# Performance work log

Hardware: AMD Instinct MI355X
Metric: run time of the kernel (lower is better)

## Reference

```python
import jax, jax.numpy as jnp
import numpy as np

B, C, H, W = 16, 64, 64, 64
HEADS = 8

def conv1x1(x, w):
    # x: [B, Cin, H, W], w: [Cout, Cin] -> [B, Cout, H, W]
    return jnp.einsum('oc,bchw->bohw', w, x)

def maxpool2x2(x):
    b, c, h, w = x.shape
    return x.reshape(b, c, h // 2, 2, w // 2, 2).max(axis=(3, 5))

def setup_inputs() -> dict:
    key = jax.random.key(0)
    ks = jax.random.split(key, 6)
    x = jax.random.normal(ks[0], (B, C, H, W), dtype=jnp.float32)
    w_theta = jax.random.normal(ks[1], (C // HEADS, C), dtype=jnp.float32) * 0.05
    w_phi = jax.random.normal(ks[2], (C // HEADS, C), dtype=jnp.float32) * 0.05
    w_g = jax.random.normal(ks[3], (C // 2, C), dtype=jnp.float32) * 0.05
    w_o = jax.random.normal(ks[4], (C, C // 2), dtype=jnp.float32) * 0.05
    gamma = jax.random.normal(ks[5], (), dtype=jnp.float32)
    return {'x': x, 'w_theta': w_theta, 'w_phi': w_phi, 'w_g': w_g, 'w_o': w_o, 'gamma': gamma}

def reference(x, w_theta, w_phi, w_g, w_o, gamma):
    b, c, h, w = x.shape
    n = h * w                      # query length
    m = n // 4                     # kv length after 2x2 maxpool
    theta = conv1x1(x, w_theta).reshape(b, c // HEADS, n)   # [B, C/h, N]
    phi = maxpool2x2(conv1x1(x, w_phi)).reshape(b, c // HEADS, m)  # [B, C/h, M]
    g = maxpool2x2(conv1x1(x, w_g)).reshape(b, c // 2, m)   # [B, C/2, M]
    # attention: theta^T @ phi -> [B, N, M]; NOTE: no 1/sqrt(d) scaling (SAGAN)
    beta = jax.nn.softmax(jnp.einsum('bdn,bdm->bnm', theta, phi), axis=-1)
    # o = g @ beta^T -> [B, C/2, N]
    o = jnp.einsum('bdm,bnm->bdn', g, beta).reshape(b, c // 2, h, w)
    o = conv1x1(o, w_o)            # [B, C, H, W]
    return gamma * o + x
```

## Files before the change

### kernel.cpp

```cpp
#include <hip/hip_runtime.h>
#include <hip/hip_bf16.h>

#define NB 16
#define NC 64
#define NN 4096
#define NM 1024
#define ND 8
#define NG 32

typedef short short8 __attribute__((ext_vector_type(8)));
typedef float floatx4 __attribute__((ext_vector_type(4)));

#define LOG2E 1.44269504f

__device__ __forceinline__ short f2bfs(float f) {
    union { __hip_bfloat16 h; short s; } u;
    u.h = __float2bfloat16(f);
    return u.s;
}
__device__ __forceinline__ unsigned pack2bf(float a, float b) {
    return (unsigned)(unsigned short)f2bfs(a) | ((unsigned)(unsigned short)f2bfs(b) << 16);
}
__device__ __forceinline__ unsigned pk2fast(float a, float b) {
    unsigned ua = __float_as_uint(a) + 0x8000u;
    unsigned ub = __float_as_uint(b) + 0x8000u;
    return __builtin_amdgcn_perm(ub, ua, 0x07060302);
}
__device__ __forceinline__ short8 u4s8(uint4 v) {
    union { uint4 u; short8 s; } c; c.u = v; return c.s;
}

__device__ __forceinline__ uint4 ld_coh(const unsigned* base, size_t u4idx) {
    const unsigned long long* p = (const unsigned long long*)base + u4idx * 2;
    unsigned long long lo = __hip_atomic_load(p,     __ATOMIC_RELAXED,
                                              __HIP_MEMORY_SCOPE_SYSTEM);
    unsigned long long hi = __hip_atomic_load(p + 1, __ATOMIC_RELAXED,
                                              __HIP_MEMORY_SCOPE_SYSTEM);
    return make_uint4((unsigned)lo, (unsigned)(lo >> 32),
                      (unsigned)hi, (unsigned)(hi >> 32));
}
__device__ __forceinline__ void st_coh(unsigned* base, size_t u4idx, uint4 v) {
    unsigned long long* p = (unsigned long long*)base + u4idx * 2;
    __hip_atomic_store(p,     (unsigned long long)v.x | ((unsigned long long)v.y << 32),
                       __ATOMIC_RELAXED, __HIP_MEMORY_SCOPE_SYSTEM);
    __hip_atomic_store(p + 1, (unsigned long long)v.z | ((unsigned long long)v.w << 32),
                       __ATOMIC_RELAXED, __HIP_MEMORY_SCOPE_SYSTEM);
}

#define KG_STEP(CPP0, CPP1, CG_)                                                         \
    {                                                                                    \
        _Pragma("unroll")                                                                \
        for (int qt = 0; qt < 2; ++qt) {                                                 \
            floatx4 s0 = __builtin_amdgcn_mfma_f32_16x16x32_bf16(                        \
                u4s8(CPP0), u4s8(tb[qt]), (floatx4)0.f, 0, 0, 0);                        \
            floatx4 s1 = __builtin_amdgcn_mfma_f32_16x16x32_bf16(                        \
                u4s8(CPP1), u4s8(tb[qt]), (floatx4)0.f, 0, 0, 0);                        \
            float e0[4], e1[4];                                                          \
            _Pragma("unroll")                                                            \
            for (int r = 0; r < 4; ++r) {                                                \
                e0[r] = __builtin_amdgcn_exp2f(s0[r]);                                   \
                e1[r] = __builtin_amdgcn_exp2f(s1[r]);                                   \
            }                                                                            \
            lsum[qt] += ((e0[0] + e0[1]) + (e0[2] + e0[3]))                              \
                      + ((e1[0] + e1[1]) + (e1[2] + e1[3]));                             \
            uint4 pb = make_uint4(pk2fast(e0[0], e0[1]), pk2fast(e0[2], e0[3]),          \
                                  pk2fast(e1[0], e1[1]), pk2fast(e1[2], e1[3]));         \
            _Pragma("unroll")                                                            \
            for (int ct = 0; ct < 4; ++ct)                                               \
                acc[qt][ct] = __builtin_amdgcn_mfma_f32_16x16x32_bf16(                   \
                    u4s8(CG_[ct]), u4s8(pb), acc[qt][ct], 0, 0, 0);                      \
        }                                                                                \
    }

__global__ void init_flags(int* __restrict__ flags)
{
    flags[threadIdx.x] = 0;
}

__global__ __launch_bounds__(256, 2)
void fused_kernel(const float* __restrict__ x,
                  const float* __restrict__ w_theta,
                  const float* __restrict__ w_phi,
                  const float* __restrict__ w_g,
                  const float* __restrict__ w_o,
                  const float* __restrict__ gamma_p,
                  unsigned* __restrict__ phi_ws,
                  unsigned* __restrict__ g2_ws,
                  int* __restrict__ flags,
                  float* __restrict__ out)
{
    __shared__ __align__(16) float smem[16096];
    float* lx   = smem;
    float* lwpT = smem + 8448;
    float* lwgT = smem + 8960;
    float* lwoT = smem + 11072;
    float* lgs  = smem + 13152;
    float* lps  = smem + 14304;
    float* lwt  = smem + 14560;
    float* lth  = smem + 15072;
    uint4* lphi = (uint4*)(smem + 8960);
    uint4* lg2  = (uint4*)(smem + 13056);
    float* ltr  = smem;

    const int blk  = blockIdx.x;
    const int xcd  = blk & 7;
    const int slot = blk >> 3;
    const int b    = xcd * 2 + (slot >> 5);
    const int ph   = slot & 31;
    const int t    = threadIdx.x;
    const int w    = t >> 6;
    const int lane = t & 63;
    const int lm   = lane & 15;
    const int quad = lane >> 4;

    for (int i = t; i < 512; i += 256) {
        lwpT[(i & 63) * 8 + (i >> 6)] = w_phi[i];
        lwt[i] = w_theta[i];
    }
    for (int i = t; i < 2048; i += 256) {
        lwgT[(i & 63) * 33 + (i >> 6)] = w_g[i];
        lwoT[(i & 31) * 65 + (i >> 5)] = w_o[i];
    }
    const float* xb = x + (size_t)b * NC * NN + (size_t)ph * 128;
    for (int idx = t; idx < 2048; idx += 256) {
        int c = idx >> 5, i4 = idx & 31;
        ((float4*)(lx + c * 132))[i4] = ((const float4*)(xb + (size_t)c * NN))[i4];
    }
    __syncthreads();

    float4 xr0[4], xr1[4];
    {
        const int l16 = t & 15;
        #pragma unroll
        for (int io = 0; io < 4; ++io) {
            int co = io * 16 + (t >> 4);
            const float* p = &lx[co * 132 + l16 * 8];
            xr0[io] = ((const float4*)p)[0];
            xr1[io] = ((const float4*)p)[1];
        }
    }

    {
        int oc = t >> 3, grp = t & 7;
        float s0[16];
        #pragma unroll
        for (int i = 0; i < 16; ++i) s0[i] = 0.f;
        const float4* xl4 = (const float4*)lx;
        #pragma unroll 4
        for (int c = 0; c < 64; ++c) {
            float4 a0 = xl4[c * 33 + 2 * grp];
            float4 a1 = xl4[c * 33 + 2 * grp + 1];
            float4 b0 = xl4[c * 33 + 16 + 2 * grp];
            float4 b1 = xl4[c * 33 + 17 + 2 * grp];
            float w0 = lwgT[c * 33 + oc];
            s0[0] = fmaf(w0, a0.x, s0[0]);  s0[1] = fmaf(w0, a0.y, s0[1]);
            s0[2] = fmaf(w0, a0.z, s0[2]);  s0[3] = fmaf(w0, a0.w, s0[3]);
            s0[4] = fmaf(w0, a1.x, s0[4]);  s0[5] = fmaf(w0, a1.y, s0[5]);
            s0[6] = fmaf(w0, a1.z, s0[6]);  s0[7] = fmaf(w0, a1.w, s0[7]);
            s0[8] = fmaf(w0, b0.x, s0[8]);  s0[9] = fmaf(w0, b0.y, s0[9]);
            s0[10] = fmaf(w0, b0.z, s0[10]); s0[11] = fmaf(w0, b0.w, s0[11]);
            s0[12] = fmaf(w0, b1.x, s0[12]); s0[13] = fmaf(w0, b1.y, s0[13]);
            s0[14] = fmaf(w0, b1.z, s0[14]); s0[15] = fmaf(w0, b1.w, s0[15]);
        }
        #pragma unroll
        for (int p = 0; p < 4; ++p)
            lgs[oc * 36 + grp * 4 + p] =
                fmaxf(fmaxf(s0[2 * p], s0[2 * p + 1]), fmaxf(s0[8 + 2 * p], s0[9 + 2 * p]));
    }

    {
        int m = t >> 3, oc = t & 7;
        float s0 = 0.f, s1 = 0.f, s2 = 0.f, s3 = 0.f;
        #pragma unroll 4
        for (int c = 0; c < 64; ++c) {
            float wv = lwpT[c * 8 + oc];
            const float* xr = &lx[c * 132];
            s0 = fmaf(wv, xr[2 * m],      s0);
            s1 = fmaf(wv, xr[2 * m + 1],  s1);
            s2 = fmaf(wv, xr[64 + 2 * m], s2);
            s3 = fmaf(wv, xr[65 + 2 * m], s3);
        }
        lps[m * 8 + oc] = fmaxf(fmaxf(s0, s1), fmaxf(s2, s3));
    }

    {
        int qi = t & 127, och = (t >> 7) * 4;
        float th4[4] = {0.f, 0.f, 0.f, 0.f};
        for (int c = 0; c < 64; ++c) {
            float xv = lx[c * 132 + qi];
            #pragma unroll
            for (int o = 0; o < 4; ++o)
                th4[o] = fmaf(lwt[(och + o) * 64 + c], xv, th4[o]);
        }
        *(float4*)&lth[qi * 8 + och] = make_float4(th4[0], th4[1], th4[2], th4[3]);
    }
    __syncthreads();

    {
        int co = t >> 2, sel = t & 3;
        int m0a = 4 * sel, m0b = 16 + 4 * sel;
        float v[8];
        #pragma unroll
        for (int mm = 0; mm < 8; ++mm) v[mm] = 0.f;
        #pragma unroll 4
        for (int c = 0; c < 32; ++c) {
            float wv = lwoT[c * 65 + co];
            float4 ga = *(const float4*)&lgs[c * 36 + m0a];
            float4 gb = *(const float4*)&lgs[c * 36 + m0b];
            v[0] = fmaf(wv, ga.x, v[0]); v[1] = fmaf(wv, ga.y, v[1]);
            v[2] = fmaf(wv, ga.z, v[2]); v[3] = fmaf(wv, ga.w, v[3]);
            v[4] = fmaf(wv, gb.x, v[4]); v[5] = fmaf(wv, gb.y, v[5]);
            v[6] = fmaf(wv, gb.z, v[6]); v[7] = fmaf(wv, gb.w, v[7]);
        }
        uint4 pk;
        pk.x = pack2bf(v[0], v[1]); pk.y = pack2bf(v[2], v[3]);
        pk.z = pack2bf(v[4], v[5]); pk.w = pack2bf(v[6], v[7]);
        int ln = (sel << 4) | (co & 15);
        st_coh(g2_ws, (((size_t)b * 4 + (co >> 4)) * 32 + ph) * 64 + ln, pk);
    }

    if (t < 32) {
        const float* pr = &lps[t * 8];
        uint4 pk;
        pk.x = pack2bf(pr[0], pr[1]); pk.y = pack2bf(pr[2], pr[3]);
        pk.z = pack2bf(pr[4], pr[5]); pk.w = pack2bf(pr[6], pr[7]);
        st_coh(phi_ws, (size_t)b * NM + ph * 32 + t, pk);
    }

    uint4 tb[2];
    #pragma unroll
    for (int qt = 0; qt < 2; ++qt) {
        const float* thp = &lth[(w * 32 + qt * 16 + lm) * 8];
        float4 a = ((const float4*)thp)[0], c4 = ((const float4*)thp)[1];
        uint4 v;
        v.x = pack2bf(a.x * LOG2E, a.y * LOG2E);
        v.y = pack2bf(a.z * LOG2E, a.w * LOG2E);
        v.z = pack2bf(c4.x * LOG2E, c4.y * LOG2E);
        v.w = pack2bf(c4.z * LOG2E, c4.w * LOG2E);
        tb[qt].x = quad == 0 ? v.x : 0u;
        tb[qt].y = quad == 0 ? v.y : 0u;
        tb[qt].z = quad == 0 ? v.z : 0u;
        tb[qt].w = quad == 0 ? v.w : 0u;
    }

    asm volatile("s_waitcnt vmcnt(0)" ::: "memory");
    __syncthreads();
    if (t == 0) {
        __hip_atomic_fetch_add(&flags[b * 32], 1, __ATOMIC_RELAXED,
                               __HIP_MEMORY_SCOPE_AGENT);
        while (__hip_atomic_load(&flags[b * 32], __ATOMIC_RELAXED,
                                 __HIP_MEMORY_SCOPE_AGENT) < 32)
            __builtin_amdgcn_s_sleep(8);
    }
    __syncthreads();

    const size_t gbase = ((size_t)b * 4 + w) * 32 * 64 + lane;
    lg2[t] = ld_coh(g2_ws, gbase);
    for (int kk = t; kk < NM; kk += 256)
        lphi[kk] = ld_coh(phi_ws, (size_t)b * NM + kk);
    __syncthreads();

    floatx4 acc[2][4];
    #pragma unroll
    for (int qt = 0; qt < 2; ++qt)
        #pragma unroll
        for (int ct = 0; ct < 4; ++ct) acc[qt][ct] = (floatx4)0.f;
    float lsum[2] = {0.f, 0.f};

    for (int kg = 0; kg < 32; ++kg) {
        if (kg < 31)
            lg2[((kg + 1) & 1) * 256 + t] = ld_coh(g2_ws, gbase + (kg + 1) * 64);

        uint4 c0 = lphi[kg * 32 + lm];
        uint4 c1 = lphi[kg * 32 + 16 + lm];
        uint4 cg[4];
        #pragma unroll
        for (int ct = 0; ct < 4; ++ct)
            cg[ct] = lg2[(kg & 1) * 256 + ct * 64 + lane];

        KG_STEP(c0, c1, cg);

        __syncthreads();
    }

    float inv[2];
    {
        float l0 = lsum[0]; l0 += __shfl_xor(l0, 16); l0 += __shfl_xor(l0, 32);
        float l1 = lsum[1]; l1 += __shfl_xor(l1, 16); l1 += __shfl_xor(l1, 32);
        inv[0] = 1.0f / l0; inv[1] = 1.0f / l1;
    }

    const float gamma = gamma_p[0];

    #pragma unroll
    for (int qt = 0; qt < 2; ++qt)
        #pragma unroll
        for (int ct = 0; ct < 4; ++ct)
            #pragma unroll
            for (int r = 0; r < 4; ++r)
                ltr[(ct * 16 + quad * 4 + r) * 140 + w * 32 + qt * 16 + lm]
                    = acc[qt][ct][r] * inv[qt];
    __syncthreads();

    {
        const int l16 = t & 15;
        #pragma unroll
        for (int io = 0; io < 4; ++io) {
            int co = io * 16 + (t >> 4);
            size_t base = ((size_t)b * NC + co) * NN + (size_t)ph * 128 + l16 * 8;
            const float* tr = &ltr[co * 140 + l16 * 8];
            float4 t0 = ((const float4*)tr)[0];
            float4 t1 = ((const float4*)tr)[1];
            float4 o0 = make_float4(fmaf(gamma, t0.x, xr0[io].x), fmaf(gamma, t0.y, xr0[io].y),
                                    fmaf(gamma, t0.z, xr0[io].z), fmaf(gamma, t0.w, xr0[io].w));
            float4 o1 = make_float4(fmaf(gamma, t1.x, xr1[io].x), fmaf(gamma, t1.y, xr1[io].y),
                                    fmaf(gamma, t1.z, xr1[io].z), fmaf(gamma, t1.w, xr1[io].w));
            *(float4*)(out + base)     = o0;
            *(float4*)(out + base + 4) = o1;
        }
    }
}

extern "C" void kernel_launch(void* const* d_in, const int* in_sizes, int n_in,
                              void* d_out, int out_size, void* d_ws, size_t ws_size,
                              hipStream_t stream)
{
    const float* x  = (const float*)d_in[0];
    const float* wt = (const float*)d_in[1];
    const float* wp = (const float*)d_in[2];
    const float* wg = (const float*)d_in[3];
    const float* wo = (const float*)d_in[4];
    const float* gm = (const float*)d_in[5];
    float* out = (float*)d_out;

    unsigned* phi_ws = (unsigned*)d_ws;
    unsigned* g2_ws  = phi_ws + (size_t)NB * NM * ND / 2;
    int* flags = (int*)((char*)d_ws + (size_t)(256 * 1024 + 2 * 1024 * 1024));

    init_flags<<<1, NB * 32, 0, stream>>>(flags);
    fused_kernel<<<NB * 32, 256, 0, stream>>>(x, wt, wp, wg, wo, gm,
                                              phi_ws, g2_ws, flags, out);
}
```

Baseline: 123.1 us.

## Deepen g2 prefetch pipeline, split g-conv over channel halves, vectorize phi loads

The attention loop now processes two key groups per iteration with double-buffered LDS holding two groups each. Global loads of g2 are issued two iterations ahead into registers, which halves the number of block barriers and hides load latency. The g projection splits the channel reduction across lane pairs, each thread computing two output channels, and combines the partial sums with a shuffle. The phi projection uses float2 LDS reads. This costs more registers and relocates the lphi and lg2 LDS regions, which could lower occupancy or introduce aliasing issues.

```diff
diff --git a/kernel.cpp b/kernel.cpp
--- a/kernel.cpp
+++ b/kernel.cpp
@@ -98,8 +98,8 @@
     float* lps  = smem + 14304;
     float* lwt  = smem + 14560;
     float* lth  = smem + 15072;
-    uint4* lphi = (uint4*)(smem + 8960);
-    uint4* lg2  = (uint4*)(smem + 13056);
+    uint4* lphi = (uint4*)smem;
+    uint4* lg2  = (uint4*)(smem + 4096);
     float* ltr  = smem;
 
     const int blk  = blockIdx.x;
@@ -141,31 +141,49 @@
     }
 
     {
-        int oc = t >> 3, grp = t & 7;
-        float s0[16];
-        #pragma unroll
-        for (int i = 0; i < 16; ++i) s0[i] = 0.f;
+        int h = t & 1, grp = (t >> 1) & 7, ocp = t >> 4;
+        float s0[32];
+        #pragma unroll
+        for (int i = 0; i < 32; ++i) s0[i] = 0.f;
         const float4* xl4 = (const float4*)lx;
+        const int cbase = h * 32;
         #pragma unroll 4
-        for (int c = 0; c < 64; ++c) {
+        for (int cc = 0; cc < 32; ++cc) {
+            int c = cbase + cc;
             float4 a0 = xl4[c * 33 + 2 * grp];
             float4 a1 = xl4[c * 33 + 2 * grp + 1];
             float4 b0 = xl4[c * 33 + 16 + 2 * grp];
             float4 b1 = xl4[c * 33 + 17 + 2 * grp];
-            float w0 = lwgT[c * 33 + oc];
-            s0[0] = fmaf(w0, a0.x, s0[0]);  s0[1] = fmaf(w0, a0.y, s0[1]);
-            s0[2] = fmaf(w0, a0.z, s0[2]);  s0[3] = fmaf(w0, a0.w, s0[3]);
-            s0[4] = fmaf(w0, a1.x, s0[4]);  s0[5] = fmaf(w0, a1.y, s0[5]);
-            s0[6] = fmaf(w0, a1.z, s0[6]);  s0[7] = fmaf(w0, a1.w, s0[7]);
-            s0[8] = fmaf(w0, b0.x, s0[8]);  s0[9] = fmaf(w0, b0.y, s0[9]);
+            float w0 = lwgT[c * 33 + ocp];
+            float w1 = lwgT[c * 33 + ocp + 16];
+            s0[0]  = fmaf(w0, a0.x, s0[0]);  s0[1]  = fmaf(w0, a0.y, s0[1]);
+            s0[2]  = fmaf(w0, a0.z, s0[2]);  s0[3]  = fmaf(w0, a0.w, s0[3]);
+            s0[4]  = fmaf(w0, a1.x, s0[4]);  s0[5]  = fmaf(w0, a1.y, s0[5]);
+            s0[6]  = fmaf(w0, a1.z, s0[6]);  s0[7]  = fmaf(w0, a1.w, s0[7]);
+            s0[8]  = fmaf(w0, b0.x, s0[8]);  s0[9]  = fmaf(w0, b0.y, s0[9]);
             s0[10] = fmaf(w0, b0.z, s0[10]); s0[11] = fmaf(w0, b0.w, s0[11]);
             s0[12] = fmaf(w0, b1.x, s0[12]); s0[13] = fmaf(w0, b1.y, s0[13]);
             s0[14] = fmaf(w0, b1.z, s0[14]); s0[15] = fmaf(w0, b1.w, s0[15]);
-        }
-        #pragma unroll
-        for (int p = 0; p < 4; ++p)
-            lgs[oc * 36 + grp * 4 + p] =
-                fmaxf(fmaxf(s0[2 * p], s0[2 * p + 1]), fmaxf(s0[8 + 2 * p], s0[9 + 2 * p]));
+            s0[16] = fmaf(w1, a0.x, s0[16]); s0[17] = fmaf(w1, a0.y, s0[17]);
+            s0[18] = fmaf(w1, a0.z, s0[18]); s0[19] = fmaf(w1, a0.w, s0[19]);
+            s0[20] = fmaf(w1, a1.x, s0[20]); s0[21] = fmaf(w1, a1.y, s0[21]);
+            s0[22] = fmaf(w1, a1.z, s0[22]); s0[23] = fmaf(w1, a1.w, s0[23]);
+            s0[24] = fmaf(w1, b0.x, s0[24]); s0[25] = fmaf(w1, b0.y, s0[25]);
+            s0[26] = fmaf(w1, b0.z, s0[26]); s0[27] = fmaf(w1, b0.w, s0[27]);
+            s0[28] = fmaf(w1, b1.x, s0[28]); s0[29] = fmaf(w1, b1.y, s0[29]);
+            s0[30] = fmaf(w1, b1.z, s0[30]); s0[31] = fmaf(w1, b1.w, s0[31]);
+        }
+        #pragma unroll
+        for (int i = 0; i < 32; ++i) s0[i] += __shfl_xor(s0[i], 1);
+        int oc = ocp + h * 16;
+        #pragma unroll
+        for (int p = 0; p < 4; ++p) {
+            float va = fmaxf(fmaxf(s0[2 * p], s0[2 * p + 1]),
+                             fmaxf(s0[8 + 2 * p], s0[9 + 2 * p]));
+            float vb = fmaxf(fmaxf(s0[16 + 2 * p], s0[17 + 2 * p]),
+                             fmaxf(s0[24 + 2 * p], s0[25 + 2 * p]));
+            lgs[oc * 36 + grp * 4 + p] = h ? vb : va;
+        }
     }
 
     {
@@ -175,10 +193,12 @@
         for (int c = 0; c < 64; ++c) {
             float wv = lwpT[c * 8 + oc];
             const float* xr = &lx[c * 132];
-            s0 = fmaf(wv, xr[2 * m],      s0);
-            s1 = fmaf(wv, xr[2 * m + 1],  s1);
-            s2 = fmaf(wv, xr[64 + 2 * m], s2);
-            s3 = fmaf(wv, xr[65 + 2 * m], s3);
+            float2 q0 = *(const float2*)(xr + 2 * m);
+            float2 q1 = *(const float2*)(xr + 64 + 2 * m);
+            s0 = fmaf(wv, q0.x, s0);
+            s1 = fmaf(wv, q0.y, s1);
+            s2 = fmaf(wv, q1.x, s2);
+            s3 = fmaf(wv, q1.y, s3);
         }
         lps[m * 8 + oc] = fmaxf(fmaxf(s0, s1), fmaxf(s2, s3));
     }
@@ -255,7 +275,13 @@
     __syncthreads();
 
     const size_t gbase = ((size_t)b * 4 + w) * 32 * 64 + lane;
-    lg2[t] = ld_coh(g2_ws, gbase);
+
+    lg2[0 * 512 + 0 * 256 + t] = ld_coh(g2_ws, gbase + 0 * 64);
+    lg2[0 * 512 + 1 * 256 + t] = ld_coh(g2_ws, gbase + 1 * 64);
+    uint4 pA0 = ld_coh(g2_ws, gbase + 2 * 64);
+    uint4 pA1 = ld_coh(g2_ws, gbase + 3 * 64);
+    uint4 pB0 = ld_coh(g2_ws, gbase + 4 * 64);
+    uint4 pB1 = ld_coh(g2_ws, gbase + 5 * 64);
     for (int kk = t; kk < NM; kk += 256)
         lphi[kk] = ld_coh(phi_ws, (size_t)b * NM + kk);
     __syncthreads();
@@ -267,19 +293,38 @@
         for (int ct = 0; ct < 4; ++ct) acc[qt][ct] = (floatx4)0.f;
     float lsum[2] = {0.f, 0.f};
 
-    for (int kg = 0; kg < 32; ++kg) {
-        if (kg < 31)
-            lg2[((kg + 1) & 1) * 256 + t] = ld_coh(g2_ws, gbase + (kg + 1) * 64);
-
-        uint4 c0 = lphi[kg * 32 + lm];
-        uint4 c1 = lphi[kg * 32 + 16 + lm];
-        uint4 cg[4];
-        #pragma unroll
-        for (int ct = 0; ct < 4; ++ct)
-            cg[ct] = lg2[(kg & 1) * 256 + ct * 64 + lane];
-
-        KG_STEP(c0, c1, cg);
-
+    for (int kgp = 0; kgp < 16; ++kgp) {
+        const int buf = (kgp & 1) * 512;
+        if (kgp < 15) {
+            const int nbuf = ((kgp & 1) ^ 1) * 512;
+            lg2[nbuf + t]       = pA0;
+            lg2[nbuf + 256 + t] = pA1;
+            pA0 = pB0; pA1 = pB1;
+            if (kgp < 13) {
+                pB0 = ld_coh(g2_ws, gbase + (size_t)(2 * kgp + 6) * 64);
+                pB1 = ld_coh(g2_ws, gbase + (size_t)(2 * kgp + 7) * 64);
+            }
+        }
+        {
+            int kg = 2 * kgp;
+            uint4 c0 = lphi[kg * 32 + lm];
+            uint4 c1 = lphi[kg * 32 + 16 + lm];
+            uint4 cg[4];
+            #pragma unroll
+            for (int ct = 0; ct < 4; ++ct)
+                cg[ct] = lg2[buf + ct * 64 + lane];
+            KG_STEP(c0, c1, cg);
+        }
+        {
+            int kg = 2 * kgp + 1;
+            uint4 c0 = lphi[kg * 32 + lm];
+            uint4 c1 = lphi[kg * 32 + 16 + lm];
+            uint4 cg[4];
+            #pragma unroll
+            for (int ct = 0; ct < 4; ++ct)
+                cg[ct] = lg2[buf + 256 + ct * 64 + lane];
+            KG_STEP(c0, c1, cg);
+        }
         __syncthreads();
     }
 
```

Result: faster. 116.9 us (-5.0%).
